# Optimization experiments

Measured on AMD Instinct MI355X. Metric: run time of the kernel, lower is better.

Reference implementation:

```python
import jax, jax.numpy as jnp
import numpy as np

ALPHA = 0.1
MARGIN = 1.0
SLOPE = 0.2  # LeakyReLU negative_slope
OFFSET = 1.0e6

def leaky(x):
    return jnp.where(x >= 0, x, SLOPE * x)

def _xavier(key, shape, gain=np.sqrt(2.0)):
    fan_out, fan_in = shape[0], shape[1]
    std = gain * np.sqrt(2.0 / (fan_in + fan_out))
    return jax.random.normal(key, shape, dtype=jnp.float32) * std

def setup_inputs() -> dict:
    key = jax.random.key(0)
    ks = jax.random.split(key, 8)
    B, F, T, D, H = 32768, 128, 32, 16, 10
    return {
        "X": jax.random.normal(ks[0], (B, F), dtype=jnp.float32),
        "affine_weights": jax.random.normal(ks[1], (T, F, D), dtype=jnp.float32),
        "W0": _xavier(ks[2], (H, D)),
        "W1": _xavier(ks[3], (H, H)),
        "W2": _xavier(ks[4], (H, H)),
        "W3": _xavier(ks[5], (H, H)),
        "Wh": _xavier(ks[6], (T, H)),
        "bh": jnp.zeros((T,), dtype=jnp.float32),
    }

def reference(X, affine_weights, W0, W1, W2, W3, Wh, bh):
    T = affine_weights.shape[0]
    # goad_transforms: x_trans [B, trans_dim, n_trans]; labels[b,t] = t (implicit)
    x_trans = jnp.einsum('bn,ant->bta', X, affine_weights)
    # ConvNet encoder, kernel_size=1 convs == per-position channel matmuls
    h = jnp.einsum('od,bdt->bot', W0, x_trans)
    for W in (W1, W2, W3):
        h = jnp.einsum('od,bdt->bot', W, leaky(h))
    rep = h                                   # [B, H, T]
    # head: LeakyReLU + Conv1d(H->T, bias=True)
    pred = jnp.einsum('oh,bht->bot', Wh, leaky(rep)) + bh[None, :, None]  # [B, T, T]
    batch_rep = jnp.transpose(rep, (0, 2, 1))  # [B, T, H]
    # CrossEntropy(reduction='none') with labels[b,t]=t -> -diag of log_softmax over class dim
    logp = jax.nn.log_softmax(pred, axis=1)
    loss_ce = -jnp.diagonal(logp, axis1=1, axis2=2)          # [B, T]
    # triplet center loss
    means = jnp.mean(batch_rep, axis=0)                       # [T, H]
    res = jnp.sum((batch_rep[:, :, None, :] - means[None, None, :, :]) ** 2, axis=-1)  # [B,T,T]
    pos = jnp.diagonal(res, axis1=1, axis2=2)                 # [B, T]
    neg = jnp.min(res + jnp.eye(T, dtype=res.dtype) * OFFSET, axis=-1)  # [B, T]
    loss_tc = jnp.mean(jnp.maximum(pos + MARGIN - neg, 0.0))  # scalar
    loss = jnp.mean(ALPHA * loss_tc + loss_ce, axis=1)        # [B]
    return batch_rep, loss
```

## Files before the change

kernel.cpp:

```cpp
#include <hip/hip_runtime.h>

typedef __attribute__((ext_vector_type(8))) short bf16x8;
typedef __attribute__((ext_vector_type(4))) float f32x4;

#define BTOT 32768
#define FDIM 128
#define TDIM 32
#define DDIM 16
#define HDIM 10
#define CDIM 320
#define ALPHA_C 0.1f
#define MARGIN_C 1.0f
#define SLOPE_C 0.2f
#define OFFSET_C 1.0e6f

#define WS_A0BF 0
#define WS_MEAN 20480
#define WS_TC   20800
#define WS_CE   20864

#define R1SZ 21504
#define LDS_TOTAL (R1SZ + 21760)

__device__ __forceinline__ float leaky(float x) { return x >= 0.f ? x : SLOPE_C * x; }

__device__ __forceinline__ unsigned short f2bf(float f) {
    unsigned int u = __float_as_uint(f);
    u += 0x7fffu + ((u >> 16) & 1u);
    return (unsigned short)(u >> 16);
}

__global__ void prep_kernel(const float* __restrict__ aw, const float* __restrict__ W0,
                            unsigned short* __restrict__ a0bf) {
    int idx = blockIdx.x * blockDim.x + threadIdx.x;
    if (idx >= CDIM * FDIM) return;
    int c = idx >> 7, n = idx & 127;
    int t = c / HDIM, o = c - t * HDIM;
    const float* a = aw + ((size_t)t * FDIM + n) * DDIM;
    const float* w = W0 + o * DDIM;
    float s = 0.f;
#pragma unroll
    for (int d = 0; d < DDIM; ++d) s += a[d] * w[d];
    a0bf[idx] = f2bf(s);
}

__global__ __launch_bounds__(256) void gemm0_fused(
    const float* __restrict__ X, const unsigned short* __restrict__ a0bf,
    const float* __restrict__ W1, const float* __restrict__ W2,
    const float* __restrict__ W3, const float* __restrict__ Wh,
    const float* __restrict__ bh,
    float* __restrict__ rep, float* __restrict__ ce_acc,
    float* __restrict__ mean_acc)
{
    __shared__ __align__(16) char ldsbuf[LDS_TOTAL];
    unsigned short (*xs)[136]  = (unsigned short (*)[136])ldsbuf;
    float          (*ys)[84]   = (float (*)[84])ldsbuf;
    unsigned short (*a0s)[136] = (unsigned short (*)[136])(ldsbuf + R1SZ);
    float          (*mpart)[80]= (float (*)[80])(ldsbuf + R1SZ);

    int tid = threadIdx.x;
    int bchunk = blockIdx.x >> 2, cchunk = blockIdx.x & 3;
    int b0 = bchunk * 64, c0 = cchunk * 80;

#pragma unroll
    for (int k = 0; k < 8; ++k) {
        int idx = tid + k * 256;
        int row = idx >> 5, col4 = idx & 31;
        float4 v = reinterpret_cast<const float4*>(X + (size_t)(b0 + row) * FDIM)[col4];
        uint2 pk;
        pk.x = (unsigned)f2bf(v.x) | ((unsigned)f2bf(v.y) << 16);
        pk.y = (unsigned)f2bf(v.z) | ((unsigned)f2bf(v.w) << 16);
        *reinterpret_cast<uint2*>(&xs[row][col4 * 4]) = pk;
    }
#pragma unroll
    for (int k = 0; k < 5; ++k) {
        int idx = tid + k * 256;
        int row = idx >> 4, j = idx & 15;
        uint4 v = reinterpret_cast<const uint4*>(a0bf + (size_t)(c0 + row) * FDIM)[j];
        *reinterpret_cast<uint4*>(&a0s[row][j * 8]) = v;
    }
    __syncthreads();

    int lane = tid & 63, w = tid >> 6;
    int r16 = lane & 15, g = lane >> 4;
    bf16x8 af[4];
#pragma unroll
    for (int s = 0; s < 4; ++s)
        af[s] = *reinterpret_cast<const bf16x8*>(&xs[w * 16 + r16][s * 32 + g * 8]);
    __syncthreads();

#pragma unroll
    for (int ct = 0; ct < 5; ++ct) {
        f32x4 acc = {0.f, 0.f, 0.f, 0.f};
#pragma unroll
        for (int s = 0; s < 4; ++s) {
            bf16x8 bfrag = *reinterpret_cast<const bf16x8*>(&a0s[ct * 16 + r16][s * 32 + g * 8]);
            acc = __builtin_amdgcn_mfma_f32_16x16x32_bf16(af[s], bfrag, acc, 0, 0, 0);
        }
#pragma unroll
        for (int r = 0; r < 4; ++r)
            ys[w * 16 + g * 4 + r][ct * 16 + r16] = acc[r];
    }
    __syncthreads();

    int t8 = tid & 7;
    int t  = cchunk * 8 + t8;
    float mgg[HDIM];
#pragma unroll
    for (int o = 0; o < HDIM; ++o) mgg[o] = 0.f;

#pragma unroll
    for (int p = 0; p < 2; ++p) {
        int bl = (tid >> 3) + p * 32;
        float* yrow = &ys[bl][t8 * HDIM];
        float h[HDIM], lh[HDIM], gg[HDIM];
#pragma unroll
        for (int q = 0; q < 5; ++q) {
            float2 v = reinterpret_cast<const float2*>(yrow)[q];
            h[2 * q] = v.x; h[2 * q + 1] = v.y;
        }
#pragma unroll
        for (int o = 0; o < HDIM; ++o) lh[o] = leaky(h[o]);
#pragma unroll
        for (int o = 0; o < HDIM; ++o) { float s = 0.f;
#pragma unroll
            for (int i = 0; i < HDIM; ++i) s += W1[o * HDIM + i] * lh[i]; gg[o] = s; }
#pragma unroll
        for (int o = 0; o < HDIM; ++o) lh[o] = leaky(gg[o]);
#pragma unroll
        for (int o = 0; o < HDIM; ++o) { float s = 0.f;
#pragma unroll
            for (int i = 0; i < HDIM; ++i) s += W2[o * HDIM + i] * lh[i]; h[o] = s; }
#pragma unroll
        for (int o = 0; o < HDIM; ++o) lh[o] = leaky(h[o]);
#pragma unroll
        for (int o = 0; o < HDIM; ++o) { float s = 0.f;
#pragma unroll
            for (int i = 0; i < HDIM; ++i) s += W3[o * HDIM + i] * lh[i]; gg[o] = s; }

#pragma unroll
        for (int q = 0; q < 5; ++q) {
            float2 v; v.x = gg[2 * q]; v.y = gg[2 * q + 1];
            reinterpret_cast<float2*>(yrow)[q] = v;
        }
#pragma unroll
        for (int o = 0; o < HDIM; ++o) mgg[o] += gg[o];

#pragma unroll
        for (int o = 0; o < HDIM; ++o) lh[o] = leaky(gg[o]);
        float m = -1e30f, se = 0.f, pt = 0.f;
#pragma unroll
        for (int o = 0; o < TDIM; ++o) {
            float s = bh[o];
#pragma unroll
            for (int i = 0; i < HDIM; ++i) s += Wh[o * HDIM + i] * lh[i];
            pt = (o == t) ? s : pt;
            float nm = fmaxf(m, s);
            se = se * __expf(m - nm) + __expf(s - nm);
            m = nm;
        }
        float ce = m + __logf(se) - pt;
        ce += __shfl_xor(ce, 1, 64);
        ce += __shfl_xor(ce, 2, 64);
        ce += __shfl_xor(ce, 4, 64);
        if (t8 == 0) atomicAdd(&ce_acc[b0 + bl], ce);
    }

#pragma unroll
    for (int o = 0; o < HDIM; ++o) mpart[tid >> 3][t8 * HDIM + o] = mgg[o];
    __syncthreads();

#pragma unroll
    for (int k = 0; k < 5; ++k) {
        int idx = tid + k * 256;
        int row = idx / 20, j = idx - row * 20;
        float4 v = *reinterpret_cast<const float4*>(&ys[row][j * 4]);
        reinterpret_cast<float4*>(rep + (size_t)(b0 + row) * CDIM + c0)[j] = v;
    }
    if (tid < 80) {
        float s = 0.f;
#pragma unroll
        for (int r = 0; r < 32; ++r) s += mpart[r][tid];
        atomicAdd(&mean_acc[c0 + tid], s);
    }
}

__global__ __launch_bounds__(256) void tc_kernel(const float* __restrict__ rep,
    const float* __restrict__ mean_acc, float* __restrict__ tc_sum)
{
    __shared__ float tile[32][CDIM];
    __shared__ float mm[CDIM];
    __shared__ float msq[TDIM];
    __shared__ float wpart[4];
    int tid = threadIdx.x;
    int b0 = blockIdx.x * 32;

    for (int i = tid; i < CDIM; i += 256) mm[i] = mean_acc[i] * (1.f / BTOT);
    const float4* src = reinterpret_cast<const float4*>(rep + (size_t)b0 * CDIM);
#pragma unroll
    for (int k = 0; k < 10; ++k) {
        int idx = tid + k * 256;
        int row = idx / 80, col4 = idx - row * 80;
        *reinterpret_cast<float4*>(&tile[row][col4 * 4]) = src[idx];
    }
    __syncthreads();
    if (tid < TDIM) {
        float s = 0.f;
#pragma unroll
        for (int h = 0; h < HDIM; ++h) { float v = mm[tid * HDIM + h]; s += v * v; }
        msq[tid] = s;
    }
    __syncthreads();

    int t = tid & 31, bg = tid >> 5;
    float rv[4][HDIM], rsq[4];
#pragma unroll
    for (int j = 0; j < 4; ++j) {
        const float* rp = &tile[bg * 4 + j][t * HDIM];
        float s = 0.f;
#pragma unroll
        for (int q = 0; q < 5; ++q) {
            float2 v = reinterpret_cast<const float2*>(rp)[q];
            rv[j][2 * q] = v.x; rv[j][2 * q + 1] = v.y;
            s += v.x * v.x + v.y * v.y;
        }
        rsq[j] = s;
    }
    float pos[4], neg[4];
#pragma unroll
    for (int j = 0; j < 4; ++j) { pos[j] = 0.f; neg[j] = 1e30f; }
#pragma unroll 4
    for (int c = 0; c < TDIM; ++c) {
        float m0[HDIM];
#pragma unroll
        for (int q = 0; q < 5; ++q) {
            float2 v = reinterpret_cast<const float2*>(&mm[c * HDIM])[q];
            m0[2 * q] = v.x; m0[2 * q + 1] = v.y;
        }
        float mq = msq[c];
        bool isT = (c == t);
#pragma unroll
        for (int j = 0; j < 4; ++j) {
            float dot = 0.f;
#pragma unroll
            for (int h = 0; h < HDIM; ++h) dot += rv[j][h] * m0[h];
            float s = rsq[j] - 2.f * dot + mq;
            if (isT) pos[j] = s;
            float s2 = isT ? s + OFFSET_C : s;
            neg[j] = fminf(neg[j], s2);
        }
    }
    float hs = 0.f;
#pragma unroll
    for (int j = 0; j < 4; ++j) hs += fmaxf(pos[j] + MARGIN_C - neg[j], 0.f);
#pragma unroll
    for (int m = 1; m < 64; m <<= 1) hs += __shfl_xor(hs, m, 64);
    int lane = tid & 63, w = tid >> 6;
    if (lane == 0) wpart[w] = hs;
    __syncthreads();
    if (tid == 0) atomicAdd(tc_sum, wpart[0] + wpart[1] + wpart[2] + wpart[3]);
}

__global__ void final_kernel(const float* __restrict__ ce_acc,
                             const float* __restrict__ tc_sum, float* __restrict__ loss)
{
    int b = blockIdx.x * blockDim.x + threadIdx.x;
    if (b < BTOT)
        loss[b] = ALPHA_C * (tc_sum[0] * (1.f / ((float)BTOT * TDIM)))
                + ce_acc[b] * (1.f / TDIM);
}

extern "C" void kernel_launch(void* const* d_in, const int* in_sizes, int n_in,
                              void* d_out, int out_size, void* d_ws, size_t ws_size,
                              hipStream_t stream) {
    const float* X  = (const float*)d_in[0];
    const float* aw = (const float*)d_in[1];
    const float* W0 = (const float*)d_in[2];
    const float* W1 = (const float*)d_in[3];
    const float* W2 = (const float*)d_in[4];
    const float* W3 = (const float*)d_in[5];
    const float* Wh = (const float*)d_in[6];
    const float* bh = (const float*)d_in[7];
    float* ws = (float*)d_ws;
    unsigned short* a0bf = (unsigned short*)(ws + WS_A0BF);
    float* mean_acc = ws + WS_MEAN;
    float* tc_sum   = ws + WS_TC;
    float* ce_acc   = ws + WS_CE;
    float* out_rep = (float*)d_out;
    float* loss = out_rep + (size_t)BTOT * TDIM * HDIM;

    hipMemsetAsync(mean_acc, 0, (384 + BTOT) * sizeof(float), stream);
    prep_kernel<<<(CDIM * FDIM) / 256, 256, 0, stream>>>(aw, W0, a0bf);
    gemm0_fused<<<2048, 256, 0, stream>>>(X, a0bf, W1, W2, W3, Wh, bh,
                                          out_rep, ce_acc, mean_acc);
    tc_kernel<<<BTOT / 32, 256, 0, stream>>>(out_rep, mean_acc, tc_sum);
    final_kernel<<<BTOT / 256, 256, 0, stream>>>(ce_acc, tc_sum, loss);
}
```

Before: 89.35 us.

## Loop over all transform chunks per block to read X once and drop CE atomics

Each block now covers 32 batch rows and loops over all four 80-column chunks, instead of splitting columns across four blocks that each re-read and re-convert X. The per-row cross-entropy is summed in registers and written once as a mean, which removes the ce atomics and the large memset. The change also uses a packed bf16 convert instruction, pads the LDS row strides, and adds a launch-bounds occupancy hint. In exchange it adds a sequential chunk loop with several barriers per chunk, a serial reload of a0bf between chunks, and MFMA work that is uneven between paired waves.

```diff
diff --git a/kernel.cpp b/kernel.cpp
--- a/kernel.cpp
+++ b/kernel.cpp
@@ -19,8 +19,10 @@
 #define WS_TC   20800
 #define WS_CE   20864
 
-#define R1SZ 21504
-#define LDS_TOTAL (R1SZ + 21760)
+#define R2OFF 10368
+#define LDS_TOTAL (R2OFF + 21760)
+#define YSROW 85
+#define MPROW 81
 
 __device__ __forceinline__ float leaky(float x) { return x >= 0.f ? x : SLOPE_C * x; }
 
@@ -44,81 +46,100 @@
     a0bf[idx] = f2bf(s);
 }
 
-__global__ __launch_bounds__(256) void gemm0_fused(
+__global__ __launch_bounds__(256, 5) void gemm0_fused(
     const float* __restrict__ X, const unsigned short* __restrict__ a0bf,
     const float* __restrict__ W1, const float* __restrict__ W2,
     const float* __restrict__ W3, const float* __restrict__ Wh,
     const float* __restrict__ bh,
-    float* __restrict__ rep, float* __restrict__ ce_acc,
+    float* __restrict__ rep, float* __restrict__ ce_mean,
     float* __restrict__ mean_acc)
 {
     __shared__ __align__(16) char ldsbuf[LDS_TOTAL];
     unsigned short (*xs)[136]  = (unsigned short (*)[136])ldsbuf;
-    float          (*ys)[84]   = (float (*)[84])ldsbuf;
-    unsigned short (*a0s)[136] = (unsigned short (*)[136])(ldsbuf + R1SZ);
-    float          (*mpart)[80]= (float (*)[80])(ldsbuf + R1SZ);
+    float* mpartf = (float*)ldsbuf;
+    unsigned short (*a0s)[136] = (unsigned short (*)[136])(ldsbuf + R2OFF);
+    float* ysf = (float*)(ldsbuf + R2OFF);
 
     int tid = threadIdx.x;
-    int bchunk = blockIdx.x >> 2, cchunk = blockIdx.x & 3;
-    int b0 = bchunk * 64, c0 = cchunk * 80;
-
-#pragma unroll
-    for (int k = 0; k < 8; ++k) {
+    int b0 = blockIdx.x * 32;
+
+#pragma unroll
+    for (int k = 0; k < 4; ++k) {
         int idx = tid + k * 256;
         int row = idx >> 5, col4 = idx & 31;
         float4 v = reinterpret_cast<const float4*>(X + (size_t)(b0 + row) * FDIM)[col4];
-        uint2 pk;
-        pk.x = (unsigned)f2bf(v.x) | ((unsigned)f2bf(v.y) << 16);
-        pk.y = (unsigned)f2bf(v.z) | ((unsigned)f2bf(v.w) << 16);
+        unsigned pk0, pk1;
+        asm("v_cvt_pk_bf16_f32 %0, %1, %2" : "=v"(pk0) : "v"(v.x), "v"(v.y));
+        asm("v_cvt_pk_bf16_f32 %0, %1, %2" : "=v"(pk1) : "v"(v.z), "v"(v.w));
+        uint2 pk; pk.x = pk0; pk.y = pk1;
         *reinterpret_cast<uint2*>(&xs[row][col4 * 4]) = pk;
     }
 #pragma unroll
     for (int k = 0; k < 5; ++k) {
         int idx = tid + k * 256;
         int row = idx >> 4, j = idx & 15;
-        uint4 v = reinterpret_cast<const uint4*>(a0bf + (size_t)(c0 + row) * FDIM)[j];
+        uint4 v = reinterpret_cast<const uint4*>(a0bf + (size_t)row * FDIM)[j];
         *reinterpret_cast<uint4*>(&a0s[row][j * 8]) = v;
     }
     __syncthreads();
 
-    int lane = tid & 63, w = tid >> 6;
+    int lane = tid & 63, w = __builtin_amdgcn_readfirstlane(tid >> 6);
     int r16 = lane & 15, g = lane >> 4;
+    int sub = w >> 1;
+    int wodd = w & 1;
     bf16x8 af[4];
 #pragma unroll
     for (int s = 0; s < 4; ++s)
-        af[s] = *reinterpret_cast<const bf16x8*>(&xs[w * 16 + r16][s * 32 + g * 8]);
-    __syncthreads();
-
-#pragma unroll
-    for (int ct = 0; ct < 5; ++ct) {
-        f32x4 acc = {0.f, 0.f, 0.f, 0.f};
-#pragma unroll
-        for (int s = 0; s < 4; ++s) {
-            bf16x8 bfrag = *reinterpret_cast<const bf16x8*>(&a0s[ct * 16 + r16][s * 32 + g * 8]);
-            acc = __builtin_amdgcn_mfma_f32_16x16x32_bf16(af[s], bfrag, acc, 0, 0, 0);
-        }
-#pragma unroll
-        for (int r = 0; r < 4; ++r)
-            ys[w * 16 + g * 4 + r][ct * 16 + r16] = acc[r];
-    }
-    __syncthreads();
-
-    int t8 = tid & 7;
-    int t  = cchunk * 8 + t8;
-    float mgg[HDIM];
-#pragma unroll
-    for (int o = 0; o < HDIM; ++o) mgg[o] = 0.f;
-
-#pragma unroll
-    for (int p = 0; p < 2; ++p) {
-        int bl = (tid >> 3) + p * 32;
-        float* yrow = &ys[bl][t8 * HDIM];
+        af[s] = *reinterpret_cast<const bf16x8*>(&xs[sub * 16 + r16][s * 32 + g * 8]);
+
+    int t8 = tid & 7, bl = tid >> 3;
+    float ce_sum = 0.f;
+
+    for (int cc = 0; cc < 4; ++cc) {
+        f32x4 acc0 = {0.f,0.f,0.f,0.f}, acc1 = {0.f,0.f,0.f,0.f}, acc2 = {0.f,0.f,0.f,0.f};
+        if (wodd == 0) {
+#pragma unroll
+            for (int s = 0; s < 4; ++s) {
+                bf16x8 bf0 = *reinterpret_cast<const bf16x8*>(&a0s[ 0 + r16][s * 32 + g * 8]);
+                bf16x8 bf1 = *reinterpret_cast<const bf16x8*>(&a0s[16 + r16][s * 32 + g * 8]);
+                bf16x8 bf2 = *reinterpret_cast<const bf16x8*>(&a0s[32 + r16][s * 32 + g * 8]);
+                acc0 = __builtin_amdgcn_mfma_f32_16x16x32_bf16(af[s], bf0, acc0, 0, 0, 0);
+                acc1 = __builtin_amdgcn_mfma_f32_16x16x32_bf16(af[s], bf1, acc1, 0, 0, 0);
+                acc2 = __builtin_amdgcn_mfma_f32_16x16x32_bf16(af[s], bf2, acc2, 0, 0, 0);
+            }
+        } else {
+#pragma unroll
+            for (int s = 0; s < 4; ++s) {
+                bf16x8 bf3 = *reinterpret_cast<const bf16x8*>(&a0s[48 + r16][s * 32 + g * 8]);
+                bf16x8 bf4 = *reinterpret_cast<const bf16x8*>(&a0s[64 + r16][s * 32 + g * 8]);
+                acc0 = __builtin_amdgcn_mfma_f32_16x16x32_bf16(af[s], bf3, acc0, 0, 0, 0);
+                acc1 = __builtin_amdgcn_mfma_f32_16x16x32_bf16(af[s], bf4, acc1, 0, 0, 0);
+            }
+        }
+        __syncthreads();
+
+        int ybase = (sub * 16 + g * 4) * YSROW + r16;
+        if (wodd == 0) {
+#pragma unroll
+            for (int r = 0; r < 4; ++r) {
+                ysf[ybase + r * YSROW +  0] = acc0[r];
+                ysf[ybase + r * YSROW + 16] = acc1[r];
+                ysf[ybase + r * YSROW + 32] = acc2[r];
+            }
+        } else {
+#pragma unroll
+            for (int r = 0; r < 4; ++r) {
+                ysf[ybase + r * YSROW + 48] = acc0[r];
+                ysf[ybase + r * YSROW + 64] = acc1[r];
+            }
+        }
+        __syncthreads();
+
+        int t = cc * 8 + t8;
+        float* yrow = ysf + bl * YSROW + t8 * HDIM;
         float h[HDIM], lh[HDIM], gg[HDIM];
 #pragma unroll
-        for (int q = 0; q < 5; ++q) {
-            float2 v = reinterpret_cast<const float2*>(yrow)[q];
-            h[2 * q] = v.x; h[2 * q + 1] = v.y;
-        }
+        for (int q = 0; q < HDIM; ++q) h[q] = yrow[q];
 #pragma unroll
         for (int o = 0; o < HDIM; ++o) lh[o] = leaky(h[o]);
 #pragma unroll
@@ -139,12 +160,9 @@
             for (int i = 0; i < HDIM; ++i) s += W3[o * HDIM + i] * lh[i]; gg[o] = s; }
 
 #pragma unroll
-        for (int q = 0; q < 5; ++q) {
-            float2 v; v.x = gg[2 * q]; v.y = gg[2 * q + 1];
-            reinterpret_cast<float2*>(yrow)[q] = v;
-        }
-#pragma unroll
-        for (int o = 0; o < HDIM; ++o) mgg[o] += gg[o];
+        for (int q = 0; q < HDIM; ++q) yrow[q] = gg[q];
+#pragma unroll
+        for (int o = 0; o < HDIM; ++o) mpartf[bl * MPROW + t8 * HDIM + o] = gg[o];
 
 #pragma unroll
         for (int o = 0; o < HDIM; ++o) lh[o] = leaky(gg[o]);
@@ -159,30 +177,39 @@
             se = se * __expf(m - nm) + __expf(s - nm);
             m = nm;
         }
-        float ce = m + __logf(se) - pt;
-        ce += __shfl_xor(ce, 1, 64);
-        ce += __shfl_xor(ce, 2, 64);
-        ce += __shfl_xor(ce, 4, 64);
-        if (t8 == 0) atomicAdd(&ce_acc[b0 + bl], ce);
-    }
-
-#pragma unroll
-    for (int o = 0; o < HDIM; ++o) mpart[tid >> 3][t8 * HDIM + o] = mgg[o];
-    __syncthreads();
-
-#pragma unroll
-    for (int k = 0; k < 5; ++k) {
-        int idx = tid + k * 256;
-        int row = idx / 20, j = idx - row * 20;
-        float4 v = *reinterpret_cast<const float4*>(&ys[row][j * 4]);
-        reinterpret_cast<float4*>(rep + (size_t)(b0 + row) * CDIM + c0)[j] = v;
-    }
-    if (tid < 80) {
-        float s = 0.f;
-#pragma unroll
-        for (int r = 0; r < 32; ++r) s += mpart[r][tid];
-        atomicAdd(&mean_acc[c0 + tid], s);
-    }
+        ce_sum += m + __logf(se) - pt;
+        __syncthreads();
+
+#pragma unroll
+        for (int k = 0; k < 10; ++k) {
+            int idx = tid + k * 256;
+            int row = idx / 80, col = idx - row * 80;
+            rep[(size_t)(b0 + row) * CDIM + cc * 80 + col] = ysf[row * YSROW + col];
+        }
+        if (tid < 80) {
+            float s = 0.f;
+#pragma unroll
+            for (int r = 0; r < 32; ++r) s += mpartf[r * MPROW + tid];
+            atomicAdd(&mean_acc[cc * 80 + tid], s);
+        }
+        if (cc < 3) {
+            __syncthreads();
+#pragma unroll
+            for (int k = 0; k < 5; ++k) {
+                int idx = tid + k * 256;
+                int row = idx >> 4, j = idx & 15;
+                uint4 v = reinterpret_cast<const uint4*>(
+                    a0bf + (size_t)((cc + 1) * 80 + row) * FDIM)[j];
+                *reinterpret_cast<uint4*>(&a0s[row][j * 8]) = v;
+            }
+            __syncthreads();
+        }
+    }
+
+    ce_sum += __shfl_xor(ce_sum, 1, 64);
+    ce_sum += __shfl_xor(ce_sum, 2, 64);
+    ce_sum += __shfl_xor(ce_sum, 4, 64);
+    if (t8 == 0) ce_mean[b0 + bl] = ce_sum * (1.f / TDIM);
 }
 
 __global__ __launch_bounds__(256) void tc_kernel(const float* __restrict__ rep,
@@ -261,13 +288,12 @@
     if (tid == 0) atomicAdd(tc_sum, wpart[0] + wpart[1] + wpart[2] + wpart[3]);
 }
 
-__global__ void final_kernel(const float* __restrict__ ce_acc,
+__global__ void final_kernel(const float* __restrict__ ce_mean,
                              const float* __restrict__ tc_sum, float* __restrict__ loss)
 {
     int b = blockIdx.x * blockDim.x + threadIdx.x;
     if (b < BTOT)
-        loss[b] = ALPHA_C * (tc_sum[0] * (1.f / ((float)BTOT * TDIM)))
-                + ce_acc[b] * (1.f / TDIM);
+        loss[b] = ALPHA_C * (tc_sum[0] * (1.f / ((float)BTOT * TDIM))) + ce_mean[b];
 }
 
 extern "C" void kernel_launch(void* const* d_in, const int* in_sizes, int n_in,
@@ -285,14 +311,14 @@
     unsigned short* a0bf = (unsigned short*)(ws + WS_A0BF);
     float* mean_acc = ws + WS_MEAN;
     float* tc_sum   = ws + WS_TC;
-    float* ce_acc   = ws + WS_CE;
+    float* ce_mean  = ws + WS_CE;
     float* out_rep = (float*)d_out;
     float* loss = out_rep + (size_t)BTOT * TDIM * HDIM;
 
-    hipMemsetAsync(mean_acc, 0, (384 + BTOT) * sizeof(float), stream);
+    hipMemsetAsync(mean_acc, 0, 384 * sizeof(float), stream);
     prep_kernel<<<(CDIM * FDIM) / 256, 256, 0, stream>>>(aw, W0, a0bf);
-    gemm0_fused<<<2048, 256, 0, stream>>>(X, a0bf, W1, W2, W3, Wh, bh,
-                                          out_rep, ce_acc, mean_acc);
+    gemm0_fused<<<BTOT / 32, 256, 0, stream>>>(X, a0bf, W1, W2, W3, Wh, bh,
+                                               out_rep, ce_mean, mean_acc);
     tc_kernel<<<BTOT / 32, 256, 0, stream>>>(out_rep, mean_acc, tc_sum);
-    final_kernel<<<BTOT / 256, 256, 0, stream>>>(ce_acc, tc_sum, loss);
-}
+    final_kernel<<<BTOT / 256, 256, 0, stream>>>(ce_mean, tc_sum, loss);
+}
```

Measured after the change: 137.1 us. 53.4% more time.
